# Kernel tuning notes

Measured on AMD Instinct MI355X. Metric: run time of the kernel, lower is better.

## Reference

```python
import jax, jax.numpy as jnp
import numpy as np

B, S, IN, HID, NH, HD, R, WIN, TK = 2, 2048, 64, 512, 8, 64, 64, 5, 16
C1, C2, C3 = 171, 171, 170  # hidden_dim split across 3 conv branches (512 = 171+171+170)


def _conv(xc, w, b, pad):
    y = jax.lax.conv_general_dilated(xc, w, window_strides=(1,), padding=[(pad, pad)],
                                     dimension_numbers=('NCH', 'OIH', 'NCH'))
    return jax.nn.relu(y + b[None, :, None])


def setup_inputs():
    key = jax.random.key(0)
    ks = jax.random.split(key, 22)
    p = lambda k, sh: jax.random.normal(k, sh, jnp.float32) * 0.05
    return {
        'x': jax.random.normal(ks[0], (B, S, IN), jnp.float32),
        'conv1_w': p(ks[1], (C1, IN, 3)), 'conv1_b': p(ks[2], (C1,)),
        'conv2_w': p(ks[3], (C2, IN, 5)), 'conv2_b': p(ks[4], (C2,)),
        'conv3_w': p(ks[5], (C3, IN, 7)), 'conv3_b': p(ks[6], (C3,)),
        'Wq': p(ks[7], (HID, HID)), 'bq': p(ks[8], (HID,)),
        'Wk': p(ks[9], (HID, HID)), 'bk': p(ks[10], (HID,)),
        'Wv': p(ks[11], (HID, HID)), 'bv': p(ks[12], (HID,)),
        'Wkp': p(ks[13], (R, HD)), 'bkp': p(ks[14], (R,)),
        'Wvp': p(ks[15], (R, HD)), 'bvp': p(ks[16], (R,)),
        'Wo': p(ks[17], (HID, HID)), 'bo': p(ks[18], (HID,)),
        'ln_g': jnp.ones((HID,), jnp.float32), 'ln_b': jnp.zeros((HID,), jnp.float32),
    }


def reference(x, conv1_w, conv1_b, conv2_w, conv2_b, conv3_w, conv3_b,
              Wq, bq, Wk, bk, Wv, bv, Wkp, bkp, Wvp, bvp, Wo, bo, ln_g, ln_b):
    # multi-scale conv front-end
    xc = x.transpose(0, 2, 1)  # [B, IN, S]
    h = jnp.concatenate([_conv(xc, conv1_w, conv1_b, 1),
                         _conv(xc, conv2_w, conv2_b, 2),
                         _conv(xc, conv3_w, conv3_b, 3)], axis=1).transpose(0, 2, 1)  # [B,S,HID]

    def heads(W_, b_):
        return (h @ W_.T + b_).reshape(B, S, NH, HD).transpose(0, 2, 1, 3)  # [B,NH,S,HD]

    Q, K, V = heads(Wq, bq), heads(Wk, bk), heads(Wv, bv)
    Kp = K @ Wkp.T + bkp  # [B,NH,S,R]
    Vp = V @ Wvp.T + bvp

    # local sliding-window attention; -inf masking reproduces the per-t boundary slicing
    hw = WIN // 2
    idx = jnp.arange(S)[:, None] + jnp.arange(-hw, hw + 1)[None, :]
    valid = (idx >= 0) & (idx < S)
    idxc = jnp.clip(idx, 0, S - 1)
    Kw = K[:, :, idxc, :]
    Vw = V[:, :, idxc, :]
    ls = jnp.einsum('bhsd,bhswd->bhsw', Q, Kw) / jnp.sqrt(jnp.float32(HD))
    ls = jnp.where(valid[None, None], ls, -jnp.inf)
    local = jnp.einsum('bhsw,bhswd->bhsd', jax.nn.softmax(ls, axis=-1), Vw)

    # top-k low-rank global attention (HD == R required by original einsum)
    gs = jnp.einsum('bhqd,bhkd->bhqk', Q, Kp) / jnp.sqrt(jnp.float32(R))  # [B,NH,S,S]
    tv, ti = jax.lax.top_k(gs, TK)
    tw = jax.nn.softmax(tv, axis=-1)  # [B,NH,S,TK]
    bi = jnp.arange(B)[:, None, None, None]
    hi = jnp.arange(NH)[None, :, None, None]
    topV = Vp[bi, hi, ti]  # [B,NH,S,TK,R]
    sp = jnp.einsum('bhqk,bhqkr->bhqr', tw, topV)
    sp = sp @ Wvp.T + bvp  # extra value_proj applied to sparse output, as in original

    out = ((local + sp) * 0.5).transpose(0, 2, 1, 3).reshape(B, S, HID)
    out = out @ Wo.T + bo
    res = out + h
    mu = res.mean(-1, keepdims=True)
    var = ((res - mu) ** 2).mean(-1, keepdims=True)
    return (res - mu) / jnp.sqrt(var + 1e-5) * ln_g + ln_b
```

## Files before the change

### kernel.cpp

```cpp
#include <hip/hip_runtime.h>
#include <hip/hip_bf16.h>

#define BB 2
#define SS 2048
#define INC 64
#define HIDN 512
#define NHH 8
#define HDD 64
#define SP 2054

typedef __attribute__((ext_vector_type(8))) short bf16x8;
typedef __attribute__((ext_vector_type(4))) float f32x4;

__device__ __forceinline__ short f2bf(float f) {
  union { __hip_bfloat16 h; short s; } u;
  u.h = __float2bfloat16(f);
  return u.s;
}
__device__ __forceinline__ float bf2f(short s) {
  return __uint_as_float(((unsigned)(unsigned short)s) << 16);
}

__global__ __launch_bounds__(256) void prep_kernel(
    const float* __restrict__ x, const float* __restrict__ w1,
    const float* __restrict__ b1, const float* __restrict__ w2,
    const float* __restrict__ b2, const float* __restrict__ w3,
    const float* __restrict__ b3, const float* __restrict__ Wq,
    const float* __restrict__ Wk_, const float* __restrict__ Wv_,
    const float* __restrict__ bq, const float* __restrict__ bk_,
    const float* __restrict__ bv_, const float* __restrict__ Wo,
    const float* __restrict__ Wkp, const float* __restrict__ Wvp,
    const float* __restrict__ bvp, short* __restrict__ Wallbf,
    float* __restrict__ ball, short* __restrict__ Wobf,
    short* __restrict__ Wkpbf, short* __restrict__ W2bf,
    float* __restrict__ cvec, short* __restrict__ xbfp,
    short* __restrict__ Wcbf, float* __restrict__ bcat) {
  int i0 = blockIdx.x * 256 + threadIdx.x;
  int stride = gridDim.x * 256;
  for (int idx = i0; idx < 786432; idx += stride) {
    float v;
    if (idx < 262144)      v = Wq[idx];
    else if (idx < 524288) v = Wk_[idx - 262144];
    else                   v = Wv_[idx - 524288];
    Wallbf[idx] = f2bf(v);
  }
  for (int idx = i0; idx < 262144; idx += stride) Wobf[idx] = f2bf(Wo[idx]);
  for (int idx = i0; idx < BB * SP * 64; idx += stride) {
    int row = idx >> 6, ci = idx & 63;
    int b = row / SP, pr = row - b * SP;
    int sg = pr - 3;
    float v = (sg >= 0 && sg < SS) ? x[(b * SS + sg) * 64 + ci] : 0.f;
    xbfp[idx] = f2bf(v);
  }
  for (int idx = i0; idx < 512 * 448; idx += stride) {
    int c = idx / 448;
    int rem = idx - c * 448;
    int t = rem >> 6, ci = rem & 63;
    float v = 0.f;
    if (c < 171) {
      int k = t - 2;
      if (k >= 0 && k < 3) v = w1[(c * 64 + ci) * 3 + k];
    } else if (c < 342) {
      int k = t - 1;
      if (k >= 0 && k < 5) v = w2[((c - 171) * 64 + ci) * 5 + k];
    } else {
      v = w3[((c - 342) * 64 + ci) * 7 + t];
    }
    Wcbf[idx] = f2bf(v);
  }
  for (int idx = i0; idx < 4096; idx += stride) {
    Wkpbf[idx] = f2bf(Wkp[idx]);
    int j = idx >> 6, d = idx & 63;
    float s = 0.f;
#pragma unroll 8
    for (int i = 0; i < 64; i++) s += Wvp[j * 64 + i] * Wvp[i * 64 + d];
    W2bf[idx] = f2bf(s);
  }
  if (i0 < 1536) {
    float v;
    if (i0 < 512)       v = bq[i0];
    else if (i0 < 1024) v = bk_[i0 - 512];
    else                v = bv_[i0 - 1024];
    ball[i0] = v;
  }
  if (i0 < 512) {
    float v;
    if (i0 < 171)      v = b1[i0];
    else if (i0 < 342) v = b2[i0 - 171];
    else               v = b3[i0 - 342];
    bcat[i0] = v;
  }
  if (i0 < 64) {
    float s = bvp[i0];
#pragma unroll 8
    for (int i = 0; i < 64; i++) s += bvp[i] * Wvp[i0 * 64 + i];
    cvec[i0] = s;
  }
}

__global__ __launch_bounds__(256, 4) void gemm_conv(
    const short* __restrict__ xbfp, const short* __restrict__ Wcbf,
    const float* __restrict__ bcat, short* __restrict__ hbf) {
  int m0 = blockIdx.x * 128;
  int n0 = blockIdx.y * 64;
  int tid = threadIdx.x;
  int wvv = tid >> 6, lane = tid & 63;
  int quad = lane >> 4, l16 = lane & 15;
  int mw = m0 + wvv * 32;
  int r0 = mw + l16, r1 = r0 + 16;
  int b0 = r0 >> 11, s0 = r0 & 2047;
  int b1 = r1 >> 11, s1 = r1 & 2047;
  const short* ap0 = xbfp + (size_t)(b0 * SP + s0) * 64 + quad * 8;
  const short* ap1 = xbfp + (size_t)(b1 * SP + s1) * 64 + quad * 8;
  const short* bp = Wcbf + (size_t)(n0 + l16) * 448 + quad * 8;
  f32x4 acc[2][4] = {};
  bf16x8 cA0 = *(const bf16x8*)ap0;
  bf16x8 cA1 = *(const bf16x8*)ap1;
  bf16x8 cB0 = *(const bf16x8*)(bp + 0 * 16 * 448);
  bf16x8 cB1 = *(const bf16x8*)(bp + 1 * 16 * 448);
  bf16x8 cB2 = *(const bf16x8*)(bp + 2 * 16 * 448);
  bf16x8 cB3 = *(const bf16x8*)(bp + 3 * 16 * 448);
#pragma unroll 2
  for (int ks = 0; ks < 14; ks++) {
    int offn = (ks + 1 < 14 ? ks + 1 : 13) * 32;
    bf16x8 nA0 = *(const bf16x8*)(ap0 + offn);
    bf16x8 nA1 = *(const bf16x8*)(ap1 + offn);
    bf16x8 nB0 = *(const bf16x8*)(bp + 0 * 16 * 448 + offn);
    bf16x8 nB1 = *(const bf16x8*)(bp + 1 * 16 * 448 + offn);
    bf16x8 nB2 = *(const bf16x8*)(bp + 2 * 16 * 448 + offn);
    bf16x8 nB3 = *(const bf16x8*)(bp + 3 * 16 * 448 + offn);
    acc[0][0] = __builtin_amdgcn_mfma_f32_16x16x32_bf16(cA0, cB0, acc[0][0], 0, 0, 0);
    acc[1][0] = __builtin_amdgcn_mfma_f32_16x16x32_bf16(cA1, cB0, acc[1][0], 0, 0, 0);
    acc[0][1] = __builtin_amdgcn_mfma_f32_16x16x32_bf16(cA0, cB1, acc[0][1], 0, 0, 0);
    acc[1][1] = __builtin_amdgcn_mfma_f32_16x16x32_bf16(cA1, cB1, acc[1][1], 0, 0, 0);
    acc[0][2] = __builtin_amdgcn_mfma_f32_16x16x32_bf16(cA0, cB2, acc[0][2], 0, 0, 0);
    acc[1][2] = __builtin_amdgcn_mfma_f32_16x16x32_bf16(cA1, cB2, acc[1][2], 0, 0, 0);
    acc[0][3] = __builtin_amdgcn_mfma_f32_16x16x32_bf16(cA0, cB3, acc[0][3], 0, 0, 0);
    acc[1][3] = __builtin_amdgcn_mfma_f32_16x16x32_bf16(cA1, cB3, acc[1][3], 0, 0, 0);
    cA0 = nA0; cA1 = nA1;
    cB0 = nB0; cB1 = nB1; cB2 = nB2; cB3 = nB3;
  }
#pragma unroll
  for (int mt = 0; mt < 2; mt++) {
#pragma unroll
    for (int r = 0; r < 4; r++) {
      int m = mw + mt * 16 + quad * 4 + r;
#pragma unroll
      for (int t = 0; t < 4; t++) {
        int n = n0 + t * 16 + l16;
        float v = fmaxf(acc[mt][t][r] + bcat[n], 0.f);
        hbf[(size_t)m * 512 + n] = f2bf(v);
      }
    }
  }
}

__global__ __launch_bounds__(256, 4) void gemm_qkv(
    const short* __restrict__ Abf, const short* __restrict__ Wbf,
    const float* __restrict__ bias, short* __restrict__ Qh,
    short* __restrict__ Kh, short* __restrict__ Vh) {
  int m0 = blockIdx.x * 128;
  int n0 = blockIdx.y * 64;
  int tid = threadIdx.x;
  int wvv = tid >> 6, lane = tid & 63;
  int quad = lane >> 4, l16 = lane & 15;
  int mw = m0 + wvv * 32;
  const short* ap0 = Abf + (size_t)(mw + l16) * 512 + quad * 8;
  const short* ap1 = ap0 + 16 * 512;
  const short* bp = Wbf + (size_t)(n0 + l16) * 512 + quad * 8;
  f32x4 acc[2][4] = {};
  bf16x8 cA0 = *(const bf16x8*)ap0;
  bf16x8 cA1 = *(const bf16x8*)ap1;
  bf16x8 cB0 = *(const bf16x8*)(bp + 0 * 16 * 512);
  bf16x8 cB1 = *(const bf16x8*)(bp + 1 * 16 * 512);
  bf16x8 cB2 = *(const bf16x8*)(bp + 2 * 16 * 512);
  bf16x8 cB3 = *(const bf16x8*)(bp + 3 * 16 * 512);
#pragma unroll 2
  for (int ks = 0; ks < 16; ks++) {
    int offn = (ks + 1 < 16 ? ks + 1 : 15) * 32;
    bf16x8 nA0 = *(const bf16x8*)(ap0 + offn);
    bf16x8 nA1 = *(const bf16x8*)(ap1 + offn);
    bf16x8 nB0 = *(const bf16x8*)(bp + 0 * 16 * 512 + offn);
    bf16x8 nB1 = *(const bf16x8*)(bp + 1 * 16 * 512 + offn);
    bf16x8 nB2 = *(const bf16x8*)(bp + 2 * 16 * 512 + offn);
    bf16x8 nB3 = *(const bf16x8*)(bp + 3 * 16 * 512 + offn);
    acc[0][0] = __builtin_amdgcn_mfma_f32_16x16x32_bf16(cA0, cB0, acc[0][0], 0, 0, 0);
    acc[1][0] = __builtin_amdgcn_mfma_f32_16x16x32_bf16(cA1, cB0, acc[1][0], 0, 0, 0);
    acc[0][1] = __builtin_amdgcn_mfma_f32_16x16x32_bf16(cA0, cB1, acc[0][1], 0, 0, 0);
    acc[1][1] = __builtin_amdgcn_mfma_f32_16x16x32_bf16(cA1, cB1, acc[1][1], 0, 0, 0);
    acc[0][2] = __builtin_amdgcn_mfma_f32_16x16x32_bf16(cA0, cB2, acc[0][2], 0, 0, 0);
    acc[1][2] = __builtin_amdgcn_mfma_f32_16x16x32_bf16(cA1, cB2, acc[1][2], 0, 0, 0);
    acc[0][3] = __builtin_amdgcn_mfma_f32_16x16x32_bf16(cA0, cB3, acc[0][3], 0, 0, 0);
    acc[1][3] = __builtin_amdgcn_mfma_f32_16x16x32_bf16(cA1, cB3, acc[1][3], 0, 0, 0);
    cA0 = nA0; cA1 = nA1;
    cB0 = nB0; cB1 = nB1; cB2 = nB2; cB3 = nB3;
  }
  int which = n0 >> 9;
  int head = (n0 >> 6) & 7;
  short* dst = which == 0 ? Qh : (which == 1 ? Kh : Vh);
  float scale = which == 0 ? 0.125f : 1.0f;
#pragma unroll
  for (int mt = 0; mt < 2; mt++) {
#pragma unroll
    for (int r = 0; r < 4; r++) {
      int m = mw + mt * 16 + quad * 4 + r;
      int bb = m >> 11, s = m & 2047;
      size_t rowoff = ((size_t)(bb * 8 + head) * 2048 + s) * 64;
#pragma unroll
      for (int t = 0; t < 4; t++) {
        int hd = t * 16 + l16;
        float v = acc[mt][t][r] + bias[n0 + hd];
        dst[rowoff + hd] = f2bf(v * scale);
      }
    }
  }
}

__global__ __launch_bounds__(256, 4) void kpvp_local_kernel(
    const short* __restrict__ Kh, const short* __restrict__ Vh,
    const short* __restrict__ Wkpbf, const float* __restrict__ bkp,
    const short* __restrict__ W2bf, const float* __restrict__ cvec,
    short* __restrict__ Kph, float* __restrict__ Vpp,
    const short* __restrict__ Qh, float* __restrict__ ctxl) {
  int tid = threadIdx.x;
  __shared__ float Sloc[4][2][16][17];
  __shared__ float wloc[4][16][8];
  if (blockIdx.x < 256) {
    int m0 = blockIdx.x * 128;
    int wvv = tid >> 6, lane = tid & 63;
    int quad = lane >> 4, l16 = lane & 15;
    int mw = m0 + wvv * 32;
    {
      const short* ap0 = Kh + (size_t)(mw + l16) * 64 + quad * 8;
      const short* ap1 = ap0 + 16 * 64;
      const short* bp = Wkpbf + l16 * 64 + quad * 8;
      bf16x8 A00 = *(const bf16x8*)ap0, A01 = *(const bf16x8*)(ap0 + 32);
      bf16x8 A10 = *(const bf16x8*)ap1, A11 = *(const bf16x8*)(ap1 + 32);
      f32x4 acc[2][4] = {};
#pragma unroll
      for (int t = 0; t < 4; t++) {
        bf16x8 B0 = *(const bf16x8*)(bp + t * 16 * 64);
        bf16x8 B1 = *(const bf16x8*)(bp + t * 16 * 64 + 32);
        acc[0][t] = __builtin_amdgcn_mfma_f32_16x16x32_bf16(A00, B0, acc[0][t], 0, 0, 0);
        acc[0][t] = __builtin_amdgcn_mfma_f32_16x16x32_bf16(A01, B1, acc[0][t], 0, 0, 0);
        acc[1][t] = __builtin_amdgcn_mfma_f32_16x16x32_bf16(A10, B0, acc[1][t], 0, 0, 0);
        acc[1][t] = __builtin_amdgcn_mfma_f32_16x16x32_bf16(A11, B1, acc[1][t], 0, 0, 0);
      }
#pragma unroll
      for (int mt = 0; mt < 2; mt++)
#pragma unroll
        for (int r = 0; r < 4; r++) {
          int m = mw + mt * 16 + quad * 4 + r;
#pragma unroll
          for (int t = 0; t < 4; t++) {
            int n = t * 16 + l16;
            Kph[(size_t)m * 64 + n] = f2bf(acc[mt][t][r] + bkp[n]);
          }
        }
    }
    {
      const short* ap0 = Vh + (size_t)(mw + l16) * 64 + quad * 8;
      const short* ap1 = ap0 + 16 * 64;
      const short* bp = W2bf + l16 * 64 + quad * 8;
      bf16x8 A00 = *(const bf16x8*)ap0, A01 = *(const bf16x8*)(ap0 + 32);
      bf16x8 A10 = *(const bf16x8*)ap1, A11 = *(const bf16x8*)(ap1 + 32);
      f32x4 acc[2][4] = {};
#pragma unroll
      for (int t = 0; t < 4; t++) {
        bf16x8 B0 = *(const bf16x8*)(bp + t * 16 * 64);
        bf16x8 B1 = *(const bf16x8*)(bp + t * 16 * 64 + 32);
        acc[0][t] = __builtin_amdgcn_mfma_f32_16x16x32_bf16(A00, B0, acc[0][t], 0, 0, 0);
        acc[0][t] = __builtin_amdgcn_mfma_f32_16x16x32_bf16(A01, B1, acc[0][t], 0, 0, 0);
        acc[1][t] = __builtin_amdgcn_mfma_f32_16x16x32_bf16(A10, B0, acc[1][t], 0, 0, 0);
        acc[1][t] = __builtin_amdgcn_mfma_f32_16x16x32_bf16(A11, B1, acc[1][t], 0, 0, 0);
      }
#pragma unroll
      for (int mt = 0; mt < 2; mt++)
#pragma unroll
        for (int r = 0; r < 4; r++) {
          int m = mw + mt * 16 + quad * 4 + r;
#pragma unroll
          for (int t = 0; t < 4; t++) {
            int n = t * 16 + l16;
            Vpp[(size_t)m * 64 + n] = acc[mt][t][r] + cvec[n];
          }
        }
    }
    return;
  }
  int wv = tid >> 6;
  int tile = (blockIdx.x - 256) * 4 + wv;
  int bh = tile >> 7;
  int q0 = (tile & 127) * 16;
  int lane = tid & 63;
  int quad = lane >> 4, l16 = lane & 15;

  const short* qbase = Qh + (size_t)(bh * 2048 + q0 + l16) * 64 + quad * 8;
  bf16x8 a0 = *(const bf16x8*)qbase;
  bf16x8 a1 = *(const bf16x8*)(qbase + 32);

  int k0a = min(max(q0 - 2 + l16, 0), 2047);
  int k1a = min(q0 + 6 + l16, 2047);
  const short* kb0 = Kh + (size_t)(bh * 2048 + k0a) * 64 + quad * 8;
  const short* kb1 = Kh + (size_t)(bh * 2048 + k1a) * 64 + quad * 8;
  bf16x8 B00 = *(const bf16x8*)kb0;
  bf16x8 B01 = *(const bf16x8*)(kb0 + 32);
  bf16x8 B10 = *(const bf16x8*)kb1;
  bf16x8 B11 = *(const bf16x8*)(kb1 + 32);
  f32x4 C0 = {0.f, 0.f, 0.f, 0.f};
  f32x4 C1 = {0.f, 0.f, 0.f, 0.f};
  C0 = __builtin_amdgcn_mfma_f32_16x16x32_bf16(a0, B00, C0, 0, 0, 0);
  C0 = __builtin_amdgcn_mfma_f32_16x16x32_bf16(a1, B01, C0, 0, 0, 0);
  C1 = __builtin_amdgcn_mfma_f32_16x16x32_bf16(a0, B10, C1, 0, 0, 0);
  C1 = __builtin_amdgcn_mfma_f32_16x16x32_bf16(a1, B11, C1, 0, 0, 0);
#pragma unroll
  for (int r = 0; r < 4; r++) {
    Sloc[wv][0][quad * 4 + r][l16] = C0[r];
    Sloc[wv][1][quad * 4 + r][l16] = C1[r];
  }
  __builtin_amdgcn_wave_barrier();
  if (lane < 16) {
    int q = lane;
    float sc[5];
    bool ok[5];
#pragma unroll
    for (int j = 0; j < 5; j++) {
      int offq = q + j - 2;
      int sg = q0 + offq;
      ok[j] = (sg >= 0 && sg < SS);
      int t = offq <= 13 ? 0 : 1;
      int col = t ? offq - 6 : offq + 2;
      sc[j] = ok[j] ? Sloc[wv][t][q][col] : -3.0e38f;
    }
    float m = -3.0e38f;
#pragma unroll
    for (int j = 0; j < 5; j++) m = fmaxf(m, sc[j]);
    float e[5], l = 0.f;
#pragma unroll
    for (int j = 0; j < 5; j++) {
      e[j] = ok[j] ? __expf(sc[j] - m) : 0.f;
      l += e[j];
    }
    float inv = 1.f / l;
#pragma unroll
    for (int j = 0; j < 5; j++) wloc[wv][q][j] = e[j] * inv;
  }
  __builtin_amdgcn_wave_barrier();
  {
    int q = lane >> 2, jb = (lane & 3) * 16;
    int s = q0 + q;
    float acc[16] = {};
#pragma unroll
    for (int j = 0; j < 5; j++) {
      int sg = s + j - 2;
      if (sg >= 0 && sg < SS) {
        float w = wloc[wv][q][j];
        const short* vr = Vh + (size_t)(bh * 2048 + sg) * 64 + jb;
#pragma unroll
        for (int u = 0; u < 16; u += 4) {
          short4 v4 = *(const short4*)(vr + u);
          acc[u + 0] += w * bf2f(v4.x);
          acc[u + 1] += w * bf2f(v4.y);
          acc[u + 2] += w * bf2f(v4.z);
          acc[u + 3] += w * bf2f(v4.w);
        }
      }
    }
    float* orow = ctxl + (size_t)(bh * 2048 + s) * 64 + jb;
#pragma unroll
    for (int u = 0; u < 16; u += 4)
      *(float4*)(orow + u) =
          make_float4(acc[u], acc[u + 1], acc[u + 2], acc[u + 3]);
  }
}

__global__ __launch_bounds__(512, 1) void global_attn(
    const short* __restrict__ Qh, const short* __restrict__ Kph,
    const float* __restrict__ Vpp, const float* __restrict__ ctxl,
    short* __restrict__ ctxcb) {
  int tid = threadIdx.x;
  int wv = tid >> 6;
  int lane = tid & 63;
  int quad = lane >> 4, l16 = lane & 15;
  int p = blockIdx.x;
  int bh = (p & 7) * 2 + ((p >> 3) & 1);
  int seg = p >> 4;
  int tile = seg * 8 + wv;
  int q0 = tile * 16;

  __shared__ short Ks[2][128][64];
  __shared__ float twl[8][16][17];
  __shared__ int   txl[8][16][17];

  const short* qbase = Qh + (size_t)(bh * 2048 + q0 + l16) * 64 + quad * 8;
  bf16x8 a0 = *(const bf16x8*)qbase;
  bf16x8 a1 = *(const bf16x8*)(qbase + 32);

  const short* kpanel = Kph + (size_t)bh * (2048 * 64);

  unsigned er[4][8];
#pragma unroll
  for (int a = 0; a < 4; a++)
#pragma unroll
    for (int j = 0; j < 8; j++) er[a][j] = 0u;

  auto insert8 = [&](unsigned (&e)[8], unsigned cand) {
    unsigned n0, n1, n2, n3, n4, n5, n6, n7;
    asm("v_max_u32 %0, %1, %2" : "=v"(n0) : "v"(e[0]), "v"(cand));
    asm("v_med3_u32 %0, %1, %2, %3" : "=v"(n1) : "v"(e[0]), "v"(e[1]), "v"(cand));
    asm("v_med3_u32 %0, %1, %2, %3" : "=v"(n2) : "v"(e[1]), "v"(e[2]), "v"(cand));
    asm("v_med3_u32 %0, %1, %2, %3" : "=v"(n3) : "v"(e[2]), "v"(e[3]), "v"(cand));
    asm("v_med3_u32 %0, %1, %2, %3" : "=v"(n4) : "v"(e[3]), "v"(e[4]), "v"(cand));
    asm("v_med3_u32 %0, %1, %2, %3" : "=v"(n5) : "v"(e[4]), "v"(e[5]), "v"(cand));
    asm("v_med3_u32 %0, %1, %2, %3" : "=v"(n6) : "v"(e[5]), "v"(e[6]), "v"(cand));
    asm("v_med3_u32 %0, %1, %2, %3" : "=v"(n7) : "v"(e[6]), "v"(e[7]), "v"(cand));
    e[0] = n0; e[1] = n1; e[2] = n2; e[3] = n3;
    e[4] = n4; e[5] = n5; e[6] = n6; e[7] = n7;
  };
  auto mkcand = [&](float s, int idxr) -> unsigned {
    unsigned u = __float_as_uint(s);
    u ^= ((unsigned)((int)u >> 31)) | 0x80000000u;
    return (u & 0xFFFFF800u) | (unsigned)idxr;
  };

  int skey = tid >> 2;
  int scol = (tid & 3) * 16;
  int ssw = (skey & 7) << 3;
  const short* gsrc = kpanel + (size_t)tid * 16;

  bf16x8 c0 = *(const bf16x8*)gsrc;
  bf16x8 c1 = *(const bf16x8*)(gsrc + 8);
  {
    short* dst = &Ks[0][skey][0];
    *(bf16x8*)(dst + (scol ^ ssw)) = c0;
    *(bf16x8*)(dst + ((scol + 8) ^ ssw)) = c1;
  }
  __syncthreads();

  int rsw = ((l16 & 7) << 3);
#pragma unroll 1
  for (int ck = 0; ck < 16; ck++) {
    int cb = ck & 1, nb = cb ^ 1;
    bf16x8 p0, p1;
    if (ck < 15) {
      const short* ng = kpanel + (size_t)(ck + 1) * 8192 + tid * 16;
      p0 = *(const bf16x8*)ng;
      p1 = *(const bf16x8*)(ng + 8);
    }
#pragma unroll
    for (int gg = 0; gg < 4; gg++) {
      int k0 = gg * 32 + l16;
      int k1 = k0 + 16;
      const short* s0 = &Ks[cb][k0][0];
      const short* s1 = &Ks[cb][k1][0];
      bf16x8 B00 = *(const bf16x8*)(s0 + ((quad * 8) ^ rsw));
      bf16x8 B01 = *(const bf16x8*)(s0 + ((quad * 8 + 32) ^ rsw));
      bf16x8 B10 = *(const bf16x8*)(s1 + ((quad * 8) ^ rsw));
      bf16x8 B11 = *(const bf16x8*)(s1 + ((quad * 8 + 32) ^ rsw));
      f32x4 C0 = {0.f, 0.f, 0.f, 0.f};
      f32x4 C1 = {0.f, 0.f, 0.f, 0.f};
      C0 = __builtin_amdgcn_mfma_f32_16x16x32_bf16(a0, B00, C0, 0, 0, 0);
      C0 = __builtin_amdgcn_mfma_f32_16x16x32_bf16(a1, B01, C0, 0, 0, 0);
      C1 = __builtin_amdgcn_mfma_f32_16x16x32_bf16(a0, B10, C1, 0, 0, 0);
      C1 = __builtin_amdgcn_mfma_f32_16x16x32_bf16(a1, B11, C1, 0, 0, 0);
      int idxr0 = 2047 - (ck * 128 + gg * 32) - l16;
      int idxr1 = idxr0 - 16;
      insert8(er[0], mkcand(C0[0], idxr0));
      insert8(er[1], mkcand(C0[1], idxr0));
      insert8(er[2], mkcand(C0[2], idxr0));
      insert8(er[3], mkcand(C0[3], idxr0));
      insert8(er[0], mkcand(C1[0], idxr1));
      insert8(er[1], mkcand(C1[1], idxr1));
      insert8(er[2], mkcand(C1[2], idxr1));
      insert8(er[3], mkcand(C1[3], idxr1));
    }
    __syncthreads();
    if (ck < 15) {
      short* dst = &Ks[nb][skey][0];
      *(bf16x8*)(dst + (scol ^ ssw)) = p0;
      *(bf16x8*)(dst + ((scol + 8) ^ ssw)) = p1;
      __syncthreads();
    }
  }

  {
    float mval[4] = {0.f, 0.f, 0.f, 0.f};
    float lsum[4] = {0.f, 0.f, 0.f, 0.f};
    float myev[4] = {0.f, 0.f, 0.f, 0.f};
    int myki[4] = {0, 0, 0, 0};
#pragma unroll
    for (int t = 0; t < 16; t++) {
#pragma unroll
      for (int a = 0; a < 4; a++) {
        unsigned w = er[a][0];
#pragma unroll
        for (int mm = 1; mm <= 8; mm <<= 1) {
          unsigned o = (unsigned)__shfl_xor((int)w, mm);
          w = w > o ? w : o;
        }
        bool pop = (er[a][0] == w);
#pragma unroll
        for (int j = 0; j < 7; j++) er[a][j] = pop ? er[a][j + 1] : er[a][j];
        er[a][7] = pop ? 0u : er[a][7];
        unsigned wb = w & 0xFFFFF800u;
        unsigned uu = (w & 0x80000000u) ? (wb ^ 0x80000000u) : ~wb;
        float sv = (w == 0u) ? -1.0e30f : __uint_as_float(uu);
        if (t == 0) mval[a] = sv;
        float ex = __expf(sv - mval[a]);
        lsum[a] += ex;
        if (l16 == t) { myev[a] = ex; myki[a] = 2047 - (int)(w & 0x7FFu); }
      }
    }
#pragma unroll
    for (int a = 0; a < 4; a++) {
      twl[wv][quad * 4 + a][l16] = myev[a] / lsum[a];
      txl[wv][quad * 4 + a][l16] = myki[a];
    }
  }
  __builtin_amdgcn_wave_barrier();

  {
    int q = lane >> 2, d0 = (lane & 3) * 16;
    int b = bh >> 3, hh = bh & 7;
    const float* vball = Vpp + (size_t)bh * (2048 * 64) + d0;
    float acc[16];
#pragma unroll
    for (int u = 0; u < 16; u++) acc[u] = 0.f;
#pragma unroll 4
    for (int j = 0; j < 16; j++) {
      float w = twl[wv][q][j];
      const float* vr = vball + (size_t)txl[wv][q][j] * 64;
#pragma unroll
      for (int u = 0; u < 16; u += 4) {
        float4 v = *(const float4*)(vr + u);
        acc[u + 0] += w * v.x;
        acc[u + 1] += w * v.y;
        acc[u + 2] += w * v.z;
        acc[u + 3] += w * v.w;
      }
    }
    int s = q0 + q;
    const float* lrow = ctxl + (size_t)(bh * 2048 + s) * 64 + d0;
    short* orow = ctxcb + (size_t)(b * 2048 + s) * 512 + hh * 64 + d0;
#pragma unroll
    for (int u = 0; u < 16; u += 4) {
      float4 lv = *(const float4*)(lrow + u);
      short4 o;
      o.x = f2bf(0.5f * (lv.x + acc[u + 0]));
      o.y = f2bf(0.5f * (lv.y + acc[u + 1]));
      o.z = f2bf(0.5f * (lv.z + acc[u + 2]));
      o.w = f2bf(0.5f * (lv.w + acc[u + 3]));
      *(short4*)(orow + u) = o;
    }
  }
}

__global__ __launch_bounds__(256, 4) void gemm_wo(
    const short* __restrict__ Abf, const short* __restrict__ Wbf,
    const float* __restrict__ bo, const short* __restrict__ hbf,
    float* __restrict__ outp) {
  int m0 = blockIdx.x * 128;
  int n0 = blockIdx.y * 64;
  int tid = threadIdx.x;
  int wvv = tid >> 6, lane = tid & 63;
  int quad = lane >> 4, l16 = lane & 15;
  int mw = m0 + wvv * 32;
  const short* ap0 = Abf + (size_t)(mw + l16) * 512 + quad * 8;
  const short* ap1 = ap0 + 16 * 512;
  const short* bp = Wbf + (size_t)(n0 + l16) * 512 + quad * 8;
  f32x4 acc[2][4] = {};
  bf16x8 cA0 = *(const bf16x8*)ap0;
  bf16x8 cA1 = *(const bf16x8*)ap1;
  bf16x8 cB0 = *(const bf16x8*)(bp + 0 * 16 * 512);
  bf16x8 cB1 = *(const bf16x8*)(bp + 1 * 16 * 512);
  bf16x8 cB2 = *(const bf16x8*)(bp + 2 * 16 * 512);
  bf16x8 cB3 = *(const bf16x8*)(bp + 3 * 16 * 512);
#pragma unroll 2
  for (int ks = 0; ks < 16; ks++) {
    int offn = (ks + 1 < 16 ? ks + 1 : 15) * 32;
    bf16x8 nA0 = *(const bf16x8*)(ap0 + offn);
    bf16x8 nA1 = *(const bf16x8*)(ap1 + offn);
    bf16x8 nB0 = *(const bf16x8*)(bp + 0 * 16 * 512 + offn);
    bf16x8 nB1 = *(const bf16x8*)(bp + 1 * 16 * 512 + offn);
    bf16x8 nB2 = *(const bf16x8*)(bp + 2 * 16 * 512 + offn);
    bf16x8 nB3 = *(const bf16x8*)(bp + 3 * 16 * 512 + offn);
    acc[0][0] = __builtin_amdgcn_mfma_f32_16x16x32_bf16(cA0, cB0, acc[0][0], 0, 0, 0);
    acc[1][0] = __builtin_amdgcn_mfma_f32_16x16x32_bf16(cA1, cB0, acc[1][0], 0, 0, 0);
    acc[0][1] = __builtin_amdgcn_mfma_f32_16x16x32_bf16(cA0, cB1, acc[0][1], 0, 0, 0);
    acc[1][1] = __builtin_amdgcn_mfma_f32_16x16x32_bf16(cA1, cB1, acc[1][1], 0, 0, 0);
    acc[0][2] = __builtin_amdgcn_mfma_f32_16x16x32_bf16(cA0, cB2, acc[0][2], 0, 0, 0);
    acc[1][2] = __builtin_amdgcn_mfma_f32_16x16x32_bf16(cA1, cB2, acc[1][2], 0, 0, 0);
    acc[0][3] = __builtin_amdgcn_mfma_f32_16x16x32_bf16(cA0, cB3, acc[0][3], 0, 0, 0);
    acc[1][3] = __builtin_amdgcn_mfma_f32_16x16x32_bf16(cA1, cB3, acc[1][3], 0, 0, 0);
    cA0 = nA0; cA1 = nA1;
    cB0 = nB0; cB1 = nB1; cB2 = nB2; cB3 = nB3;
  }
#pragma unroll
  for (int mt = 0; mt < 2; mt++) {
#pragma unroll
    for (int r = 0; r < 4; r++) {
      int m = mw + mt * 16 + quad * 4 + r;
#pragma unroll
      for (int t = 0; t < 4; t++) {
        int n = n0 + t * 16 + l16;
        outp[(size_t)m * 512 + n] =
            acc[mt][t][r] + bo[n] + bf2f(hbf[(size_t)m * 512 + n]);
      }
    }
  }
}

__global__ __launch_bounds__(256) void ln_kernel(float* __restrict__ o,
                                                 const float* __restrict__ g,
                                                 const float* __restrict__ bb) {
  int row = blockIdx.x;
  int tid = threadIdx.x;
  float v0 = o[row * 512 + tid];
  float v1 = o[row * 512 + 256 + tid];
  float s = v0 + v1;
  float s2 = v0 * v0 + v1 * v1;
#pragma unroll
  for (int off = 1; off < 64; off <<= 1) {
    s += __shfl_xor(s, off);
    s2 += __shfl_xor(s2, off);
  }
  __shared__ float ps[4], ps2[4];
  int w = tid >> 6;
  if ((tid & 63) == 0) { ps[w] = s; ps2[w] = s2; }
  __syncthreads();
  float S = ps[0] + ps[1] + ps[2] + ps[3];
  float S2 = ps2[0] + ps2[1] + ps2[2] + ps2[3];
  float mu = S * (1.f / 512.f);
  float var = S2 * (1.f / 512.f) - mu * mu;
  float inv = rsqrtf(var + 1e-5f);
  o[row * 512 + tid] = (v0 - mu) * inv * g[tid] + bb[tid];
  o[row * 512 + 256 + tid] = (v1 - mu) * inv * g[tid + 256] + bb[tid + 256];
}

extern "C" void kernel_launch(void* const* d_in, const int* in_sizes, int n_in,
                              void* d_out, int out_size, void* d_ws,
                              size_t ws_size, hipStream_t stream) {
  const float* x   = (const float*)d_in[0];
  const float* w1  = (const float*)d_in[1];
  const float* b1  = (const float*)d_in[2];
  const float* w2  = (const float*)d_in[3];
  const float* b2  = (const float*)d_in[4];
  const float* w3  = (const float*)d_in[5];
  const float* b3  = (const float*)d_in[6];
  const float* Wq  = (const float*)d_in[7];
  const float* bq  = (const float*)d_in[8];
  const float* Wk  = (const float*)d_in[9];
  const float* bk  = (const float*)d_in[10];
  const float* Wv  = (const float*)d_in[11];
  const float* bv  = (const float*)d_in[12];
  const float* Wkp = (const float*)d_in[13];
  const float* bkp = (const float*)d_in[14];
  const float* Wvp = (const float*)d_in[15];
  const float* bvp = (const float*)d_in[16];
  const float* Wo  = (const float*)d_in[17];
  const float* bo  = (const float*)d_in[18];
  const float* lng = (const float*)d_in[19];
  const float* lnb = (const float*)d_in[20];

  float* p = (float*)d_ws;
  short* Wallbf = (short*)p;  p += 786432;
  float* ball   = p;          p += 2048;
  short* Wobf   = (short*)p;  p += 262144;
  short* Wkpbf  = (short*)p;  p += 4096;
  short* W2bf   = (short*)p;  p += 4096;
  float* cvec   = p;          p += 64;
  short* xbfp   = (short*)p;  p += 262912;
  short* Wcbf   = (short*)p;  p += 229376;
  float* bcat   = p;          p += 512;
  short* hbf    = (short*)p;  p += 1048576;
  short* Qh     = (short*)p;  p += 1048576;
  short* Kh     = (short*)p;  p += 1048576;
  short* Vh     = (short*)p;  p += 1048576;
  short* Kph    = (short*)p;  p += 1048576;
  float* Vpp    = p;          p += 2097152;
  float* ctxl   = p;          p += 2097152;
  short* ctxcb  = (short*)p;  p += 1048576;
  float* outF   = (float*)d_out;

  prep_kernel<<<512, 256, 0, stream>>>(x, w1, b1, w2, b2, w3, b3, Wq, Wk, Wv,
                                       bq, bk, bv, Wo, Wkp, Wvp, bvp, Wallbf,
                                       ball, Wobf, Wkpbf, W2bf, cvec, xbfp,
                                       Wcbf, bcat);
  {
    dim3 g(32, 8);
    gemm_conv<<<g, 256, 0, stream>>>(xbfp, Wcbf, bcat, hbf);
  }
  {
    dim3 g(32, 24);
    gemm_qkv<<<g, 256, 0, stream>>>(hbf, Wallbf, ball, Qh, Kh, Vh);
  }
  kpvp_local_kernel<<<768, 256, 0, stream>>>(Kh, Vh, Wkpbf, bkp, W2bf, cvec,
                                             Kph, Vpp, Qh, ctxl);
  global_attn<<<256, 512, 0, stream>>>(Qh, Kph, Vpp, ctxl, ctxcb);
  {
    dim3 g(32, 8);
    gemm_wo<<<g, 256, 0, stream>>>(ctxcb, Wobf, bo, hbf, outF);
  }
  ln_kernel<<<4096, 256, 0, stream>>>(outF, lng, lnb);
}
```

Baseline: 239.8 us.

## Store Kp in MFMA fragment layout and read it directly in global attention

The Kp projection now writes its output in a layout that matches the MFMA B-operand fragments, so each lane of the global attention kernel can load its operand straight from global memory with one vector load. The LDS double-buffered staging of K panels and its block barriers are removed. Blocks shrink from 512 to 256 threads and the grid doubles, with launch bounds allowing four blocks per CU for higher occupancy. In exchange, every wave re-reads the full Kp panel from global memory or cache instead of sharing it through LDS, which raises L2 traffic.

```diff
diff --git a/kernel.cpp b/kernel.cpp
--- a/kernel.cpp
+++ b/kernel.cpp
@@ -220,7 +220,7 @@
     const short* __restrict__ Kh, const short* __restrict__ Vh,
     const short* __restrict__ Wkpbf, const float* __restrict__ bkp,
     const short* __restrict__ W2bf, const float* __restrict__ cvec,
-    short* __restrict__ Kph, float* __restrict__ Vpp,
+    short* __restrict__ Kfrag, float* __restrict__ Vpp,
     const short* __restrict__ Qh, float* __restrict__ ctxl) {
   int tid = threadIdx.x;
   __shared__ float Sloc[4][2][16][17];
@@ -251,10 +251,14 @@
 #pragma unroll
         for (int r = 0; r < 4; r++) {
           int m = mw + mt * 16 + quad * 4 + r;
+          int m15 = m & 15;
+          size_t gbase = (size_t)(m >> 4) * 1024;
 #pragma unroll
           for (int t = 0; t < 4; t++) {
             int n = t * 16 + l16;
-            Kph[(size_t)m * 64 + n] = f2bf(acc[mt][t][r] + bkp[n]);
+            short val = f2bf(acc[mt][t][r] + bkp[n]);
+            Kfrag[gbase + (size_t)(n >> 5) * 512 +
+                  ((((n & 31) >> 3) * 16 + m15) << 3) + (n & 7)] = val;
           }
         }
     }
@@ -374,8 +378,8 @@
   }
 }
 
-__global__ __launch_bounds__(512, 1) void global_attn(
-    const short* __restrict__ Qh, const short* __restrict__ Kph,
+__global__ __launch_bounds__(256, 4) void global_attn(
+    const short* __restrict__ Qh, const short* __restrict__ Kfrag,
     const float* __restrict__ Vpp, const float* __restrict__ ctxl,
     short* __restrict__ ctxcb) {
   int tid = threadIdx.x;
@@ -385,18 +389,17 @@
   int p = blockIdx.x;
   int bh = (p & 7) * 2 + ((p >> 3) & 1);
   int seg = p >> 4;
-  int tile = seg * 8 + wv;
+  int tile = seg * 4 + wv;
   int q0 = tile * 16;
 
-  __shared__ short Ks[2][128][64];
-  __shared__ float twl[8][16][17];
-  __shared__ int   txl[8][16][17];
+  __shared__ float twl[4][16][17];
+  __shared__ int   txl[4][16][17];
 
   const short* qbase = Qh + (size_t)(bh * 2048 + q0 + l16) * 64 + quad * 8;
   bf16x8 a0 = *(const bf16x8*)qbase;
   bf16x8 a1 = *(const bf16x8*)(qbase + 32);
 
-  const short* kpanel = Kph + (size_t)bh * (2048 * 64);
+  const short* kf = Kfrag + (size_t)bh * (128 * 1024) + lane * 8;
 
   unsigned er[4][8];
 #pragma unroll
@@ -423,64 +426,19 @@
     return (u & 0xFFFFF800u) | (unsigned)idxr;
   };
 
-  int skey = tid >> 2;
-  int scol = (tid & 3) * 16;
-  int ssw = (skey & 7) << 3;
-  const short* gsrc = kpanel + (size_t)tid * 16;
-
-  bf16x8 c0 = *(const bf16x8*)gsrc;
-  bf16x8 c1 = *(const bf16x8*)(gsrc + 8);
-  {
-    short* dst = &Ks[0][skey][0];
-    *(bf16x8*)(dst + (scol ^ ssw)) = c0;
-    *(bf16x8*)(dst + ((scol + 8) ^ ssw)) = c1;
-  }
-  __syncthreads();
-
-  int rsw = ((l16 & 7) << 3);
-#pragma unroll 1
-  for (int ck = 0; ck < 16; ck++) {
-    int cb = ck & 1, nb = cb ^ 1;
-    bf16x8 p0, p1;
-    if (ck < 15) {
-      const short* ng = kpanel + (size_t)(ck + 1) * 8192 + tid * 16;
-      p0 = *(const bf16x8*)ng;
-      p1 = *(const bf16x8*)(ng + 8);
-    }
-#pragma unroll
-    for (int gg = 0; gg < 4; gg++) {
-      int k0 = gg * 32 + l16;
-      int k1 = k0 + 16;
-      const short* s0 = &Ks[cb][k0][0];
-      const short* s1 = &Ks[cb][k1][0];
-      bf16x8 B00 = *(const bf16x8*)(s0 + ((quad * 8) ^ rsw));
-      bf16x8 B01 = *(const bf16x8*)(s0 + ((quad * 8 + 32) ^ rsw));
-      bf16x8 B10 = *(const bf16x8*)(s1 + ((quad * 8) ^ rsw));
-      bf16x8 B11 = *(const bf16x8*)(s1 + ((quad * 8 + 32) ^ rsw));
-      f32x4 C0 = {0.f, 0.f, 0.f, 0.f};
-      f32x4 C1 = {0.f, 0.f, 0.f, 0.f};
-      C0 = __builtin_amdgcn_mfma_f32_16x16x32_bf16(a0, B00, C0, 0, 0, 0);
-      C0 = __builtin_amdgcn_mfma_f32_16x16x32_bf16(a1, B01, C0, 0, 0, 0);
-      C1 = __builtin_amdgcn_mfma_f32_16x16x32_bf16(a0, B10, C1, 0, 0, 0);
-      C1 = __builtin_amdgcn_mfma_f32_16x16x32_bf16(a1, B11, C1, 0, 0, 0);
-      int idxr0 = 2047 - (ck * 128 + gg * 32) - l16;
-      int idxr1 = idxr0 - 16;
-      insert8(er[0], mkcand(C0[0], idxr0));
-      insert8(er[1], mkcand(C0[1], idxr0));
-      insert8(er[2], mkcand(C0[2], idxr0));
-      insert8(er[3], mkcand(C0[3], idxr0));
-      insert8(er[0], mkcand(C1[0], idxr1));
-      insert8(er[1], mkcand(C1[1], idxr1));
-      insert8(er[2], mkcand(C1[2], idxr1));
-      insert8(er[3], mkcand(C1[3], idxr1));
-    }
-    __syncthreads();
-    if (ck < 15) {
-      short* dst = &Ks[nb][skey][0];
-      *(bf16x8*)(dst + (scol ^ ssw)) = p0;
-      *(bf16x8*)(dst + ((scol + 8) ^ ssw)) = p1;
-      __syncthreads();
-    }
+  int idxb = 2047 - l16;
+#pragma unroll 4
+  for (int g = 0; g < 128; g++) {
+    bf16x8 B00 = *(const bf16x8*)(kf + g * 1024);
+    bf16x8 B01 = *(const bf16x8*)(kf + g * 1024 + 512);
+    f32x4 C0 = {0.f, 0.f, 0.f, 0.f};
+    C0 = __builtin_amdgcn_mfma_f32_16x16x32_bf16(a0, B00, C0, 0, 0, 0);
+    C0 = __builtin_amdgcn_mfma_f32_16x16x32_bf16(a1, B01, C0, 0, 0, 0);
+    int idxr = idxb - (g << 4);
+    insert8(er[0], mkcand(C0[0], idxr));
+    insert8(er[1], mkcand(C0[1], idxr));
+    insert8(er[2], mkcand(C0[2], idxr));
+    insert8(er[3], mkcand(C0[3], idxr));
   }
 
   {
@@ -676,7 +634,7 @@
   short* Qh     = (short*)p;  p += 1048576;
   short* Kh     = (short*)p;  p += 1048576;
   short* Vh     = (short*)p;  p += 1048576;
-  short* Kph    = (short*)p;  p += 1048576;
+  short* Kfrag  = (short*)p;  p += 1048576;
   float* Vpp    = p;          p += 2097152;
   float* ctxl   = p;          p += 2097152;
   short* ctxcb  = (short*)p;  p += 1048576;
@@ -695,8 +653,8 @@
     gemm_qkv<<<g, 256, 0, stream>>>(hbf, Wallbf, ball, Qh, Kh, Vh);
   }
   kpvp_local_kernel<<<768, 256, 0, stream>>>(Kh, Vh, Wkpbf, bkp, W2bf, cvec,
-                                             Kph, Vpp, Qh, ctxl);
-  global_attn<<<256, 512, 0, stream>>>(Qh, Kph, Vpp, ctxl, ctxcb);
+                                             Kfrag, Vpp, Qh, ctxl);
+  global_attn<<<512, 256, 0, stream>>>(Qh, Kfrag, Vpp, ctxl, ctxcb);
   {
     dim3 g(32, 8);
     gemm_wo<<<g, 256, 0, stream>>>(ctxcb, Wobf, bo, hbf, outF);
```

Result: faster. 230.2 us (-4.0%).
